# Kernel optimization log

Hardware: AMD Instinct MI355X
Metric: run time of the kernel (lower is better)

Reference implementation:

```python
import jax, jax.numpy as jnp
import numpy as np

N_VOCAB_TOTAL = 32064  # n_vocab + n_nts
D_MODEL = 256


def setup_inputs() -> dict:
    key = jax.random.key(0)
    ks = jax.random.split(key, 8)
    d = D_MODEL
    tokens = jax.random.randint(ks[0], (64, 4095), 0, N_VOCAB_TOTAL, dtype=jnp.int32)
    # embedding_tgt: normal with std 1/sqrt(d) (reset_parameters)
    E = jax.random.normal(ks[1], (N_VOCAB_TOTAL, d), dtype=jnp.float32) / jnp.sqrt(jnp.float32(d))
    s_in = 1.0 / np.sqrt(3 * d)
    s_h = 1.0 / np.sqrt(d)
    W_in = jax.random.uniform(ks[2], (d, 3 * d), jnp.float32, -s_in, s_in)  # Linear(3d, d)
    b_in = jax.random.uniform(ks[3], (d,), jnp.float32, -s_in, s_in)
    W1 = jax.random.uniform(ks[4], (d, d), jnp.float32, -s_h, s_h)
    b1 = jax.random.uniform(ks[5], (d,), jnp.float32, -s_h, s_h)
    W2 = jax.random.uniform(ks[6], (d, d), jnp.float32, -s_h, s_h)
    b2 = jax.random.uniform(ks[7], (d,), jnp.float32, -s_h, s_h)
    return {"tokens": tokens, "E": E, "W_in": W_in, "b_in": b_in,
            "W1": W1, "b1": b1, "W2": W2, "b2": b2}


def _bin_agg(roots, left, right, W_in, b_in, W1, b1, W2, b2):
    # skipmlp_binary_agg: root + hidden(inp(cat([root,left,right])))
    # hidden = ELU -> Linear -> ELU -> Linear  (nlayers=2)
    x = jnp.concatenate([roots, left, right], axis=-1)        # [..., 3d]
    h = x @ W_in.T + b_in                                     # inp: Linear(3d, d)
    h = jax.nn.elu(h) @ W1.T + b1
    h = jax.nn.elu(h) @ W2.T + b2
    return roots + h


def reference(tokens, E, W_in, b_in, W1, b1, W2, b2):
    # tokens: [B, N] heap-ordered perfect binary trees, N = 2^(D+1)-1.
    B, N = tokens.shape
    n_leaves = (N + 1) // 2
    emb = E[tokens]                                           # [B, N, d] gather
    cur = emb[:, N - n_leaves:]                               # leaf level, [B, 2^D, d]
    level = n_leaves // 2
    while level >= 1:                                          # fixed D iterations
        roots = emb[:, level - 1: 2 * level - 1]               # [B, level, d]
        left = cur[:, 0::2]
        right = cur[:, 1::2]
        cur = _bin_agg(roots, left, right, W_in, b_in, W1, b1, W2, b2)
        level //= 2
    return cur[:, 0]                                           # [B, d] root embeddings
```

## Files before the change

### kernel.cpp

```cpp
#include <hip/hip_runtime.h>
#include <stdint.h>


typedef __attribute__((ext_vector_type(8))) short short8;
typedef __attribute__((ext_vector_type(4))) float f32x4;

#define XS_STRIDE 264
#define TOK_N 4095

__device__ __forceinline__ unsigned short f32_to_bf16(float f) {
    union { float f; unsigned u; } v; v.f = f;
    return (unsigned short)((v.u + 0x7fffu + ((v.u >> 16) & 1u)) >> 16);
}
__device__ __forceinline__ float bf16_to_f32(unsigned short u) {
    union { unsigned u; float f; } v; v.u = ((unsigned)u) << 16; return v.f;
}

__global__ void convert_f32_bf16(const float* __restrict__ E,
                                 const float* __restrict__ Win,
                                 const float* __restrict__ W1,
                                 const float* __restrict__ W2,
                                 unsigned short* __restrict__ Ebf,
                                 unsigned short* __restrict__ Winbf,
                                 unsigned short* __restrict__ W1bf,
                                 unsigned short* __restrict__ W2bf) {
    const int nE = 32064 * 256, nWin = 256 * 768, nW = 256 * 256;
    const int total4 = (nE + nWin + 2 * nW) >> 2;
    for (int i = blockIdx.x * blockDim.x + threadIdx.x; i < total4;
         i += gridDim.x * blockDim.x) {
        int idx = i << 2;
        const float* src; unsigned short* dst; int off;
        if (idx < nE)                  { src = E;   dst = Ebf;   off = idx; }
        else if (idx < nE + nWin)      { src = Win; dst = Winbf; off = idx - nE; }
        else if (idx < nE + nWin + nW) { src = W1;  dst = W1bf;  off = idx - nE - nWin; }
        else                           { src = W2;  dst = W2bf;  off = idx - nE - nWin - nW; }
        float4 f = *(const float4*)(src + off);
        ushort4 o;
        o.x = f32_to_bf16(f.x); o.y = f32_to_bf16(f.y);
        o.z = f32_to_bf16(f.z); o.w = f32_to_bf16(f.w);
        *(ushort4*)(dst + off) = o;
    }
}

template<int MT>
__global__ __launch_bounds__(256, (MT == 8) ? 2 : 4)
void tree_level(const int* __restrict__ tokens,
                const unsigned short* __restrict__ Ebf,
                const unsigned short* __restrict__ Win,
                const unsigned short* __restrict__ W1,
                const unsigned short* __restrict__ W2,
                const float* __restrict__ b_in,
                const float* __restrict__ b1,
                const float* __restrict__ b2,
                const unsigned short* __restrict__ cur_in,
                unsigned short* __restrict__ cur_out,
                float* __restrict__ final_out,
                int L, int logL, int first, int last)
{
    constexpr int R = MT * 16;
    constexpr int GITER = R / 8;
    constexpr bool PF = (MT < 8);
    extern __shared__ unsigned short Xs[];

    const int tid  = threadIdx.x;
    const int lane = tid & 63;
    const int wid  = tid >> 6;
    const int l15  = lane & 15;
    const int q    = lane >> 4;
    const int n0   = wid * 64;
    const int blk  = blockIdx.x;
    const int c    = tid & 31;
    const int sub  = tid >> 5;

    auto gsrc = [&](int p, int r) -> const unsigned short* {
        int g = blk * R + r;
        int b = g >> logL;
        int i = g - (b << logL);
        if (p == 0) {
            int tok = tokens[b * TOK_N + (L - 1) + i];
            return Ebf + (size_t)tok * 256;
        } else if (first) {
            int tok = tokens[b * TOK_N + 2047 + 2 * i + (p - 1)];
            return Ebf + (size_t)tok * 256;
        } else {
            return cur_in + ((size_t)b * (2 * L) + 2 * i + (p - 1)) * 256;
        }
    };

    auto stage = [&](int p) {
        short8 t[GITER];
#pragma unroll
        for (int it = 0; it < GITER; ++it)
            t[it] = *(const short8*)(gsrc(p, it * 8 + sub) + c * 8);
#pragma unroll
        for (int it = 0; it < GITER; ++it)
            *(short8*)(&Xs[(it * 8 + sub) * XS_STRIDE + c * 8]) = t[it];
    };

    f32x4 acc[MT][4];

    auto run_gemm = [&](const unsigned short* base, int nstride, int kbase) {
        short8 bb[2][4];
#pragma unroll
        for (int k = 0; k < 2; ++k)
#pragma unroll
            for (int nt = 0; nt < 4; ++nt)
                bb[k][nt] = *(const short8*)(base + (size_t)(nt * 16) * nstride + kbase + k * 32);
#pragma unroll
        for (int k = 0; k < 8; ++k) {
            short8 a[MT];
#pragma unroll
            for (int mt = 0; mt < MT; ++mt)
                a[mt] = *(const short8*)(&Xs[(mt * 16 + l15) * XS_STRIDE + k * 32 + q * 8]);
#pragma unroll
            for (int mt = 0; mt < MT; ++mt)
#pragma unroll
                for (int nt = 0; nt < 4; ++nt)
                    acc[mt][nt] = __builtin_amdgcn_mfma_f32_16x16x32_bf16(
                        a[mt], bb[k & 1][nt], acc[mt][nt], 0, 0, 0);
            if (k + 2 < 8) {
#pragma unroll
                for (int nt = 0; nt < 4; ++nt)
                    bb[k & 1][nt] = *(const short8*)(base + (size_t)(nt * 16) * nstride + kbase + (k + 2) * 32);
            }
        }
    };

    auto acc_init = [&](const float* __restrict__ b) {
        float bv[4];
#pragma unroll
        for (int nt = 0; nt < 4; ++nt) bv[nt] = b[n0 + nt * 16 + l15];
#pragma unroll
        for (int mt = 0; mt < MT; ++mt)
#pragma unroll
            for (int nt = 0; nt < 4; ++nt)
                acc[mt][nt] = (f32x4){bv[nt], bv[nt], bv[nt], bv[nt]};
    };

    auto elu_to_Xs = [&]() {
#pragma unroll
        for (int mt = 0; mt < MT; ++mt)
#pragma unroll
            for (int nt = 0; nt < 4; ++nt)
#pragma unroll
                for (int r = 0; r < 4; ++r) {
                    float h = acc[mt][nt][r];
                    h = h > 0.f ? h : (__expf(h) - 1.f);
                    Xs[(mt * 16 + q * 4 + r) * XS_STRIDE + n0 + nt * 16 + l15] = f32_to_bf16(h);
                }
    };

    short8 g[PF ? GITER : 1];

    if constexpr (PF) {
#pragma unroll
        for (int it = 0; it < GITER; ++it)
            g[it] = *(const short8*)(gsrc(0, it * 8 + sub) + c * 8);
#pragma unroll
        for (int it = 0; it < GITER; ++it)
            *(short8*)(&Xs[(it * 8 + sub) * XS_STRIDE + c * 8]) = g[it];
    } else {
        stage(0);
    }
    __syncthreads();

    acc_init(b_in);
    const unsigned short* wbase = Win + q * 8 + (size_t)(n0 + l15) * 768;
    for (int p = 0; p < 3; ++p) {
        if constexpr (PF) {
            if (p < 2) {
#pragma unroll
                for (int it = 0; it < GITER; ++it)
                    g[it] = *(const short8*)(gsrc(p + 1, it * 8 + sub) + c * 8);
            }
        }
        run_gemm(wbase, 768, p * 256);
        __syncthreads();
        if (p < 2) {
            if constexpr (PF) {
#pragma unroll
                for (int it = 0; it < GITER; ++it)
                    *(short8*)(&Xs[(it * 8 + sub) * XS_STRIDE + c * 8]) = g[it];
            } else {
                stage(p + 1);
            }
            __syncthreads();
        }
    }

    elu_to_Xs();
    __syncthreads();

    acc_init(b1);
    if constexpr (PF) {
#pragma unroll
        for (int it = 0; it < GITER; ++it)
            g[it] = *(const short8*)(gsrc(0, it * 8 + sub) + c * 8);
    }
    run_gemm(W1 + q * 8 + (size_t)(n0 + l15) * 256, 256, 0);
    __syncthreads();

    elu_to_Xs();
    __syncthreads();

    acc_init(b2);
    run_gemm(W2 + q * 8 + (size_t)(n0 + l15) * 256, 256, 0);
    __syncthreads();
    if constexpr (PF) {
#pragma unroll
        for (int it = 0; it < GITER; ++it)
            *(short8*)(&Xs[(it * 8 + sub) * XS_STRIDE + c * 8]) = g[it];
    } else {
        stage(0);
    }
    __syncthreads();

    if (last) {
#pragma unroll
        for (int mt = 0; mt < MT; ++mt)
#pragma unroll
            for (int r = 0; r < 4; ++r) {
                int row = mt * 16 + q * 4 + r;
                int gg  = blk * R + row;
#pragma unroll
                for (int nt = 0; nt < 4; ++nt) {
                    int col = n0 + nt * 16 + l15;
                    float o = acc[mt][nt][r] + bf16_to_f32(Xs[row * XS_STRIDE + col]);
                    final_out[(size_t)gg * 256 + col] = o;
                }
            }
    } else {
#pragma unroll
        for (int mt = 0; mt < MT; ++mt)
#pragma unroll
            for (int r = 0; r < 4; ++r) {
                int row = mt * 16 + q * 4 + r;
#pragma unroll
                for (int nt = 0; nt < 4; ++nt) {
                    int col = n0 + nt * 16 + l15;
                    float o = acc[mt][nt][r] + bf16_to_f32(Xs[row * XS_STRIDE + col]);
                    Xs[row * XS_STRIDE + col] = f32_to_bf16(o);
                }
            }
        __syncthreads();
#pragma unroll
        for (int it = 0; it < GITER; ++it) {
            int row = it * 8 + sub;
            *(short8*)(cur_out + ((size_t)(blk * R + row)) * 256 + c * 8) =
                *(const short8*)(&Xs[row * XS_STRIDE + c * 8]);
        }
    }
}

extern "C" void kernel_launch(void* const* d_in, const int* in_sizes, int n_in,
                              void* d_out, int out_size, void* d_ws, size_t ws_size,
                              hipStream_t stream) {
    const int*   tokens = (const int*)  d_in[0];
    const float* E      = (const float*)d_in[1];
    const float* W_in   = (const float*)d_in[2];
    const float* b_in   = (const float*)d_in[3];
    const float* W1     = (const float*)d_in[4];
    const float* b1     = (const float*)d_in[5];
    const float* W2     = (const float*)d_in[6];
    const float* b2     = (const float*)d_in[7];
    float* out = (float*)d_out;
    char* ws = (char*)d_ws;

    unsigned short* Ebf   = (unsigned short*)(ws);
    unsigned short* Winbf = (unsigned short*)(ws + 16416768);
    unsigned short* W1bf  = (unsigned short*)(ws + 16809984);
    unsigned short* W2bf  = (unsigned short*)(ws + 16941056);
    unsigned short* curA  = (unsigned short*)(ws + 17072128);
    unsigned short* curB  = (unsigned short*)(ws + 50626560);

    static bool attr_done = false;
    if (!attr_done) {
        void (*kfn)(const int*, const unsigned short*, const unsigned short*,
                    const unsigned short*, const unsigned short*, const float*,
                    const float*, const float*, const unsigned short*,
                    unsigned short*, float*, int, int, int, int) = tree_level<8>;
        (void)hipFuncSetAttribute(reinterpret_cast<const void*>(kfn),
                                  hipFuncAttributeMaxDynamicSharedMemorySize,
                                  128 * XS_STRIDE * 2);
        attr_done = true;
    }

    convert_f32_bf16<<<1024, 256, 0, stream>>>(E, W_in, W1, W2,
                                               Ebf, Winbf, W1bf, W2bf);

    const unsigned short* cin = curA;
    unsigned short* cout = curA;
    int first = 1;
    for (int L = 1024; L >= 1; L >>= 1) {
        int logL = 31 - __builtin_clz((unsigned)L);
        int last = (L == 1);
        int MTs = (L >= 512) ? 8 : (L == 256 ? 2 : 1);
        int R = 16 * MTs;
        int blocks = (64 * L) / R;
        size_t shmem = (size_t)R * XS_STRIDE * 2;
        if (MTs == 8)
            tree_level<8><<<dim3(blocks), dim3(256), shmem, stream>>>(
                tokens, Ebf, Winbf, W1bf, W2bf, b_in, b1, b2,
                cin, last ? nullptr : cout, last ? out : nullptr, L, logL, first, last);
        else if (MTs == 2)
            tree_level<2><<<dim3(blocks), dim3(256), shmem, stream>>>(
                tokens, Ebf, Winbf, W1bf, W2bf, b_in, b1, b2,
                cin, last ? nullptr : cout, last ? out : nullptr, L, logL, first, last);
        else
            tree_level<1><<<dim3(blocks), dim3(256), shmem, stream>>>(
                tokens, Ebf, Winbf, W1bf, W2bf, b_in, b1, b2,
                cin, last ? nullptr : cout, last ? out : nullptr, L, logL, first, last);
        cin = cout;
        cout = (cout == curA) ? curB : curA;
        first = 0;
    }
}
```

Before: 475.1 us.

## Fuse small tree levels into one per-tree persistent kernel using LDS intermediates

Replaces the per-level launches for levels 128 down to 1 with a single kernel where each block processes one batch tree through all remaining levels, keeping intermediate node embeddings in shared memory. This removes several kernel launches and global memory round-trips for tiny levels. In exchange only 64 blocks run and every level computes a full 128-row tile even when few rows are valid, wasting matrix work. Helper lambdas are also hoisted into templated device functions.

```diff
diff --git a/kernel.cpp b/kernel.cpp
--- a/kernel.cpp
+++ b/kernel.cpp
@@ -43,6 +43,68 @@
 }
 
 template<int MT>
+__device__ __forceinline__ void acc_bias_init(f32x4 (&acc)[MT][4],
+                                              const float* __restrict__ b,
+                                              int n0, int l15) {
+    float bv[4];
+#pragma unroll
+    for (int nt = 0; nt < 4; ++nt) bv[nt] = b[n0 + nt * 16 + l15];
+#pragma unroll
+    for (int mt = 0; mt < MT; ++mt)
+#pragma unroll
+        for (int nt = 0; nt < 4; ++nt)
+            acc[mt][nt] = (f32x4){bv[nt], bv[nt], bv[nt], bv[nt]};
+}
+
+template<int MT>
+__device__ __forceinline__ void mfma_gemm(const unsigned short* Xs,
+                                          f32x4 (&acc)[MT][4],
+                                          const unsigned short* __restrict__ base,
+                                          int nstride, int kbase,
+                                          int l15, int q) {
+    short8 bb[2][4];
+#pragma unroll
+    for (int k = 0; k < 2; ++k)
+#pragma unroll
+        for (int nt = 0; nt < 4; ++nt)
+            bb[k][nt] = *(const short8*)(base + (size_t)(nt * 16) * nstride + kbase + k * 32);
+#pragma unroll
+    for (int k = 0; k < 8; ++k) {
+        short8 a[MT];
+#pragma unroll
+        for (int mt = 0; mt < MT; ++mt)
+            a[mt] = *(const short8*)(&Xs[(mt * 16 + l15) * XS_STRIDE + k * 32 + q * 8]);
+#pragma unroll
+        for (int mt = 0; mt < MT; ++mt)
+#pragma unroll
+            for (int nt = 0; nt < 4; ++nt)
+                acc[mt][nt] = __builtin_amdgcn_mfma_f32_16x16x32_bf16(
+                    a[mt], bb[k & 1][nt], acc[mt][nt], 0, 0, 0);
+        if (k + 2 < 8) {
+#pragma unroll
+            for (int nt = 0; nt < 4; ++nt)
+                bb[k & 1][nt] = *(const short8*)(base + (size_t)(nt * 16) * nstride + kbase + (k + 2) * 32);
+        }
+    }
+}
+
+template<int MT>
+__device__ __forceinline__ void elu_store_Xs(unsigned short* Xs,
+                                             f32x4 (&acc)[MT][4],
+                                             int n0, int l15, int q) {
+#pragma unroll
+    for (int mt = 0; mt < MT; ++mt)
+#pragma unroll
+        for (int nt = 0; nt < 4; ++nt)
+#pragma unroll
+            for (int r = 0; r < 4; ++r) {
+                float h = acc[mt][nt][r];
+                h = h > 0.f ? h : (__expf(h) - 1.f);
+                Xs[(mt * 16 + q * 4 + r) * XS_STRIDE + n0 + nt * 16 + l15] = f32_to_bf16(h);
+            }
+}
+
+template<int MT>
 __global__ __launch_bounds__(256, (MT == 8) ? 2 : 4)
 void tree_level(const int* __restrict__ tokens,
                 const unsigned short* __restrict__ Ebf,
@@ -54,8 +116,7 @@
                 const float* __restrict__ b2,
                 const unsigned short* __restrict__ cur_in,
                 unsigned short* __restrict__ cur_out,
-                float* __restrict__ final_out,
-                int L, int logL, int first, int last)
+                int L, int logL, int first)
 {
     constexpr int R = MT * 16;
     constexpr int GITER = R / 8;
@@ -98,58 +159,6 @@
     };
 
     f32x4 acc[MT][4];
-
-    auto run_gemm = [&](const unsigned short* base, int nstride, int kbase) {
-        short8 bb[2][4];
-#pragma unroll
-        for (int k = 0; k < 2; ++k)
-#pragma unroll
-            for (int nt = 0; nt < 4; ++nt)
-                bb[k][nt] = *(const short8*)(base + (size_t)(nt * 16) * nstride + kbase + k * 32);
-#pragma unroll
-        for (int k = 0; k < 8; ++k) {
-            short8 a[MT];
-#pragma unroll
-            for (int mt = 0; mt < MT; ++mt)
-                a[mt] = *(const short8*)(&Xs[(mt * 16 + l15) * XS_STRIDE + k * 32 + q * 8]);
-#pragma unroll
-            for (int mt = 0; mt < MT; ++mt)
-#pragma unroll
-                for (int nt = 0; nt < 4; ++nt)
-                    acc[mt][nt] = __builtin_amdgcn_mfma_f32_16x16x32_bf16(
-                        a[mt], bb[k & 1][nt], acc[mt][nt], 0, 0, 0);
-            if (k + 2 < 8) {
-#pragma unroll
-                for (int nt = 0; nt < 4; ++nt)
-                    bb[k & 1][nt] = *(const short8*)(base + (size_t)(nt * 16) * nstride + kbase + (k + 2) * 32);
-            }
-        }
-    };
-
-    auto acc_init = [&](const float* __restrict__ b) {
-        float bv[4];
-#pragma unroll
-        for (int nt = 0; nt < 4; ++nt) bv[nt] = b[n0 + nt * 16 + l15];
-#pragma unroll
-        for (int mt = 0; mt < MT; ++mt)
-#pragma unroll
-            for (int nt = 0; nt < 4; ++nt)
-                acc[mt][nt] = (f32x4){bv[nt], bv[nt], bv[nt], bv[nt]};
-    };
-
-    auto elu_to_Xs = [&]() {
-#pragma unroll
-        for (int mt = 0; mt < MT; ++mt)
-#pragma unroll
-            for (int nt = 0; nt < 4; ++nt)
-#pragma unroll
-                for (int r = 0; r < 4; ++r) {
-                    float h = acc[mt][nt][r];
-                    h = h > 0.f ? h : (__expf(h) - 1.f);
-                    Xs[(mt * 16 + q * 4 + r) * XS_STRIDE + n0 + nt * 16 + l15] = f32_to_bf16(h);
-                }
-    };
-
     short8 g[PF ? GITER : 1];
 
     if constexpr (PF) {
@@ -164,7 +173,7 @@
     }
     __syncthreads();
 
-    acc_init(b_in);
+    acc_bias_init<MT>(acc, b_in, n0, l15);
     const unsigned short* wbase = Win + q * 8 + (size_t)(n0 + l15) * 768;
     for (int p = 0; p < 3; ++p) {
         if constexpr (PF) {
@@ -174,7 +183,7 @@
                     g[it] = *(const short8*)(gsrc(p + 1, it * 8 + sub) + c * 8);
             }
         }
-        run_gemm(wbase, 768, p * 256);
+        mfma_gemm<MT>(Xs, acc, wbase, 768, p * 256, l15, q);
         __syncthreads();
         if (p < 2) {
             if constexpr (PF) {
@@ -188,23 +197,23 @@
         }
     }
 
-    elu_to_Xs();
-    __syncthreads();
-
-    acc_init(b1);
+    elu_store_Xs<MT>(Xs, acc, n0, l15, q);
+    __syncthreads();
+
+    acc_bias_init<MT>(acc, b1, n0, l15);
     if constexpr (PF) {
 #pragma unroll
         for (int it = 0; it < GITER; ++it)
             g[it] = *(const short8*)(gsrc(0, it * 8 + sub) + c * 8);
     }
-    run_gemm(W1 + q * 8 + (size_t)(n0 + l15) * 256, 256, 0);
-    __syncthreads();
-
-    elu_to_Xs();
-    __syncthreads();
-
-    acc_init(b2);
-    run_gemm(W2 + q * 8 + (size_t)(n0 + l15) * 256, 256, 0);
+    mfma_gemm<MT>(Xs, acc, W1 + q * 8 + (size_t)(n0 + l15) * 256, 256, 0, l15, q);
+    __syncthreads();
+
+    elu_store_Xs<MT>(Xs, acc, n0, l15, q);
+    __syncthreads();
+
+    acc_bias_init<MT>(acc, b2, n0, l15);
+    mfma_gemm<MT>(Xs, acc, W2 + q * 8 + (size_t)(n0 + l15) * 256, 256, 0, l15, q);
     __syncthreads();
     if constexpr (PF) {
 #pragma unroll
@@ -215,40 +224,139 @@
     }
     __syncthreads();
 
-    if (last) {
-#pragma unroll
-        for (int mt = 0; mt < MT; ++mt)
-#pragma unroll
-            for (int r = 0; r < 4; ++r) {
-                int row = mt * 16 + q * 4 + r;
-                int gg  = blk * R + row;
-#pragma unroll
-                for (int nt = 0; nt < 4; ++nt) {
-                    int col = n0 + nt * 16 + l15;
-                    float o = acc[mt][nt][r] + bf16_to_f32(Xs[row * XS_STRIDE + col]);
-                    final_out[(size_t)gg * 256 + col] = o;
+#pragma unroll
+    for (int mt = 0; mt < MT; ++mt)
+#pragma unroll
+        for (int r = 0; r < 4; ++r) {
+            int row = mt * 16 + q * 4 + r;
+#pragma unroll
+            for (int nt = 0; nt < 4; ++nt) {
+                int col = n0 + nt * 16 + l15;
+                float o = acc[mt][nt][r] + bf16_to_f32(Xs[row * XS_STRIDE + col]);
+                Xs[row * XS_STRIDE + col] = f32_to_bf16(o);
+            }
+        }
+    __syncthreads();
+#pragma unroll
+    for (int it = 0; it < GITER; ++it) {
+        int row = it * 8 + sub;
+        *(short8*)(cur_out + ((size_t)(blk * R + row)) * 256 + c * 8) =
+            *(const short8*)(&Xs[row * XS_STRIDE + c * 8]);
+    }
+}
+
+__global__ __launch_bounds__(256, 2)
+void tree_tail(const int* __restrict__ tokens,
+               const unsigned short* __restrict__ Ebf,
+               const unsigned short* __restrict__ Win,
+               const unsigned short* __restrict__ W1,
+               const unsigned short* __restrict__ W2,
+               const float* __restrict__ b_in,
+               const float* __restrict__ b1,
+               const float* __restrict__ b2,
+               const unsigned short* __restrict__ cur_in,
+               float* __restrict__ final_out)
+{
+    constexpr int MT = 8;
+    constexpr int GITER = 16;
+    extern __shared__ unsigned short lds[];
+    unsigned short* Xs = lds;
+    unsigned short* Pv = lds + 128 * XS_STRIDE;
+
+    const int tid  = threadIdx.x;
+    const int lane = tid & 63;
+    const int wid  = tid >> 6;
+    const int l15  = lane & 15;
+    const int q    = lane >> 4;
+    const int n0   = wid * 64;
+    const int b    = blockIdx.x;
+    const int c    = tid & 31;
+    const int sub  = tid >> 5;
+
+    f32x4 acc[MT][4];
+
+    for (int L = 128; L >= 1; L >>= 1) {
+        const int Lm = L - 1;
+
+        auto src = [&](int p, int i) -> const unsigned short* {
+            int il = i & Lm;
+            if (p == 0) {
+                int tok = tokens[b * TOK_N + (L - 1) + il];
+                return Ebf + (size_t)tok * 256;
+            }
+            if (L == 128)
+                return cur_in + ((size_t)b * 256 + 2 * il + (p - 1)) * 256;
+            return Pv + (2 * il + (p - 1)) * 256;
+        };
+        auto stg = [&](int p) {
+            short8 t[GITER];
+#pragma unroll
+            for (int it = 0; it < GITER; ++it)
+                t[it] = *(const short8*)(src(p, it * 8 + sub) + c * 8);
+#pragma unroll
+            for (int it = 0; it < GITER; ++it)
+                *(short8*)(&Xs[(it * 8 + sub) * XS_STRIDE + c * 8]) = t[it];
+        };
+
+        stg(0);
+        __syncthreads();
+
+        acc_bias_init<MT>(acc, b_in, n0, l15);
+        const unsigned short* wbase = Win + q * 8 + (size_t)(n0 + l15) * 768;
+        for (int p = 0; p < 3; ++p) {
+            mfma_gemm<MT>(Xs, acc, wbase, 768, p * 256, l15, q);
+            __syncthreads();
+            if (p < 2) { stg(p + 1); __syncthreads(); }
+        }
+
+        elu_store_Xs<MT>(Xs, acc, n0, l15, q);
+        __syncthreads();
+
+        acc_bias_init<MT>(acc, b1, n0, l15);
+        mfma_gemm<MT>(Xs, acc, W1 + q * 8 + (size_t)(n0 + l15) * 256, 256, 0, l15, q);
+        __syncthreads();
+
+        elu_store_Xs<MT>(Xs, acc, n0, l15, q);
+        __syncthreads();
+
+        acc_bias_init<MT>(acc, b2, n0, l15);
+        mfma_gemm<MT>(Xs, acc, W2 + q * 8 + (size_t)(n0 + l15) * 256, 256, 0, l15, q);
+        __syncthreads();
+        stg(0);
+        __syncthreads();
+
+        if (L == 1) {
+#pragma unroll
+            for (int mt = 0; mt < MT; ++mt)
+#pragma unroll
+                for (int r = 0; r < 4; ++r) {
+                    int row = mt * 16 + q * 4 + r;
+                    if (row == 0) {
+#pragma unroll
+                        for (int nt = 0; nt < 4; ++nt) {
+                            int col = n0 + nt * 16 + l15;
+                            final_out[(size_t)b * 256 + col] =
+                                acc[mt][nt][r] + bf16_to_f32(Xs[row * XS_STRIDE + col]);
+                        }
+                    }
                 }
-            }
-    } else {
-#pragma unroll
-        for (int mt = 0; mt < MT; ++mt)
-#pragma unroll
-            for (int r = 0; r < 4; ++r) {
-                int row = mt * 16 + q * 4 + r;
-#pragma unroll
-                for (int nt = 0; nt < 4; ++nt) {
-                    int col = n0 + nt * 16 + l15;
-                    float o = acc[mt][nt][r] + bf16_to_f32(Xs[row * XS_STRIDE + col]);
-                    Xs[row * XS_STRIDE + col] = f32_to_bf16(o);
+        } else {
+#pragma unroll
+            for (int mt = 0; mt < MT; ++mt)
+#pragma unroll
+                for (int r = 0; r < 4; ++r) {
+                    int row = mt * 16 + q * 4 + r;
+                    if (row < L) {
+#pragma unroll
+                        for (int nt = 0; nt < 4; ++nt) {
+                            int col = n0 + nt * 16 + l15;
+                            float o = acc[mt][nt][r] + bf16_to_f32(Xs[row * XS_STRIDE + col]);
+                            Pv[row * 256 + col] = f32_to_bf16(o);
+                        }
+                    }
                 }
-            }
-        __syncthreads();
-#pragma unroll
-        for (int it = 0; it < GITER; ++it) {
-            int row = it * 8 + sub;
-            *(short8*)(cur_out + ((size_t)(blk * R + row)) * 256 + c * 8) =
-                *(const short8*)(&Xs[row * XS_STRIDE + c * 8]);
-        }
+        }
+        __syncthreads();
     }
 }
 
@@ -275,43 +383,31 @@
 
     static bool attr_done = false;
     if (!attr_done) {
-        void (*kfn)(const int*, const unsigned short*, const unsigned short*,
-                    const unsigned short*, const unsigned short*, const float*,
-                    const float*, const float*, const unsigned short*,
-                    unsigned short*, float*, int, int, int, int) = tree_level<8>;
-        (void)hipFuncSetAttribute(reinterpret_cast<const void*>(kfn),
+        void (*k8)(const int*, const unsigned short*, const unsigned short*,
+                   const unsigned short*, const unsigned short*, const float*,
+                   const float*, const float*, const unsigned short*,
+                   unsigned short*, int, int, int) = tree_level<8>;
+        (void)hipFuncSetAttribute(reinterpret_cast<const void*>(k8),
                                   hipFuncAttributeMaxDynamicSharedMemorySize,
                                   128 * XS_STRIDE * 2);
+        (void)hipFuncSetAttribute(reinterpret_cast<const void*>(&tree_tail),
+                                  hipFuncAttributeMaxDynamicSharedMemorySize,
+                                  128 * XS_STRIDE * 2 + 128 * 256 * 2);
         attr_done = true;
     }
 
     convert_f32_bf16<<<1024, 256, 0, stream>>>(E, W_in, W1, W2,
                                                Ebf, Winbf, W1bf, W2bf);
 
-    const unsigned short* cin = curA;
-    unsigned short* cout = curA;
-    int first = 1;
-    for (int L = 1024; L >= 1; L >>= 1) {
-        int logL = 31 - __builtin_clz((unsigned)L);
-        int last = (L == 1);
-        int MTs = (L >= 512) ? 8 : (L == 256 ? 2 : 1);
-        int R = 16 * MTs;
-        int blocks = (64 * L) / R;
-        size_t shmem = (size_t)R * XS_STRIDE * 2;
-        if (MTs == 8)
-            tree_level<8><<<dim3(blocks), dim3(256), shmem, stream>>>(
-                tokens, Ebf, Winbf, W1bf, W2bf, b_in, b1, b2,
-                cin, last ? nullptr : cout, last ? out : nullptr, L, logL, first, last);
-        else if (MTs == 2)
-            tree_level<2><<<dim3(blocks), dim3(256), shmem, stream>>>(
-                tokens, Ebf, Winbf, W1bf, W2bf, b_in, b1, b2,
-                cin, last ? nullptr : cout, last ? out : nullptr, L, logL, first, last);
-        else
-            tree_level<1><<<dim3(blocks), dim3(256), shmem, stream>>>(
-                tokens, Ebf, Winbf, W1bf, W2bf, b_in, b1, b2,
-                cin, last ? nullptr : cout, last ? out : nullptr, L, logL, first, last);
-        cin = cout;
-        cout = (cout == curA) ? curB : curA;
-        first = 0;
-    }
-}
+    tree_level<8><<<dim3(512), dim3(256), 128 * XS_STRIDE * 2, stream>>>(
+        tokens, Ebf, Winbf, W1bf, W2bf, b_in, b1, b2,
+        nullptr, curA, 1024, 10, 1);
+    tree_level<8><<<dim3(256), dim3(256), 128 * XS_STRIDE * 2, stream>>>(
+        tokens, Ebf, Winbf, W1bf, W2bf, b_in, b1, b2,
+        curA, curB, 512, 9, 0);
+    tree_level<2><<<dim3(512), dim3(256), 32 * XS_STRIDE * 2, stream>>>(
+        tokens, Ebf, Winbf, W1bf, W2bf, b_in, b1, b2,
+        curB, curA, 256, 8, 0);
+    tree_tail<<<dim3(64), dim3(256), 128 * XS_STRIDE * 2 + 128 * 256 * 2, stream>>>(
+        tokens, Ebf, Winbf, W1bf, W2bf, b_in, b1, b2, curA, out);
+}
```

After: 770.0 us. 62.1% more time.
